# Performance work log

Measured on AMD Instinct MI355X. Metric: run time of the kernel, lower is better.

The kernel has to match this reference:

```python
import jax, jax.numpy as jnp
import numpy as np

N_NODES = 100000
N_EDGES = 1600000
IN_DIM, HID_DIM, OUT_DIM = 128, 64, 64


def setup_inputs() -> dict:
    key = jax.random.key(0)
    k1, k2, k3, k4, k5, k6 = jax.random.split(key, 6)
    x = jax.random.normal(k1, (N_NODES, IN_DIM), dtype=jnp.float32)
    edge_index = jax.random.randint(k2, (2, N_EDGES), 0, N_NODES, dtype=jnp.int64)
    s1 = (2.0 / (IN_DIM + HID_DIM)) ** 0.5
    s2 = (2.0 / (HID_DIM + OUT_DIM)) ** 0.5
    W1 = jax.random.normal(k3, (IN_DIM, HID_DIM), dtype=jnp.float32) * s1
    b1 = jnp.zeros((HID_DIM,), dtype=jnp.float32)
    W2 = jax.random.normal(k4, (HID_DIM, OUT_DIM), dtype=jnp.float32) * s2
    b2 = jnp.zeros((OUT_DIM,), dtype=jnp.float32)
    return {"x": x, "edge_index": edge_index, "W1": W1, "b1": b1, "W2": W2, "b2": b2}


def _gcn_conv(x, src, dst, W, b, num_nodes):
    # linear transform then gather-normalize-scatter (GCN symmetric norm, self-loops added)
    h = x @ W  # [N, F]
    loop = jnp.arange(num_nodes, dtype=src.dtype)
    s = jnp.concatenate([src, loop])
    d = jnp.concatenate([dst, loop])
    ones = jnp.ones(s.shape[0], dtype=h.dtype)
    deg = jax.ops.segment_sum(ones, d, num_segments=num_nodes)
    dinv = jnp.where(deg > 0, jax.lax.rsqrt(jnp.maximum(deg, 1.0)), 0.0)
    norm = dinv[s] * dinv[d]  # [E+N]
    msg = h[s] * norm[:, None]  # gather + scale
    out = jax.ops.segment_sum(msg, d, num_segments=num_nodes)  # scatter-add
    return out + b


def reference(x, edge_index, W1, b1, W2, b2):
    src, dst = edge_index[0], edge_index[1]
    h = jax.nn.relu(_gcn_conv(x, src, dst, W1, b1, N_NODES))
    out = _gcn_conv(h, src, dst, W2, b2, N_NODES)
    return out
```

## Files before the change

kernel.cpp:

```cpp
#include <hip/hip_runtime.h>
#include <hip/hip_bf16.h>


#define FDIM 64
#define NPB  128
#define MAXB1 800

static __device__ __forceinline__ unsigned short f2bf(float f) {
    unsigned int u = __float_as_uint(f);
    unsigned int r = 0x7FFFu + ((u >> 16) & 1u);
    return (unsigned short)((u + r) >> 16);
}
static __device__ __forceinline__ float lof(unsigned int u) {
    return __uint_as_float(u << 16);
}
static __device__ __forceinline__ float hif(unsigned int u) {
    return __uint_as_float(u & 0xFFFF0000u);
}

__global__ __launch_bounds__(256) void bucket_hist(const int* __restrict__ dst, int E,
                                                   int B1, int chunk, int B0,
                                                   int* __restrict__ H) {
    __shared__ int hist[MAXB1];
    const int blk = blockIdx.x, t = threadIdx.x;
    for (int i = t; i < B1; i += 256) hist[i] = 0;
    __syncthreads();
    const int beg = blk * chunk, end = min(E, beg + chunk);
    for (int e = beg + t; e < end; e += 256) atomicAdd(&hist[dst[e] >> 7], 1);
    __syncthreads();
    for (int i = t; i < B1; i += 256) H[i * B0 + blk] = hist[i];
}

__global__ __launch_bounds__(256) void scanA(const int* __restrict__ a, int S,
                                             int* __restrict__ bs) {
    __shared__ int s[256];
    const int blk = blockIdx.x, t = threadIdx.x;
    const int base = blk * 2048 + t * 8;
    int sum = 0;
    #pragma unroll
    for (int j = 0; j < 8; ++j) { int idx = base + j; if (idx < S) sum += a[idx]; }
    s[t] = sum;
    __syncthreads();
    for (int off = 128; off > 0; off >>= 1) {
        if (t < off) s[t] += s[t + off];
        __syncthreads();
    }
    if (t == 0) bs[blk] = s[0];
}

__global__ __launch_bounds__(512) void scanB(int* __restrict__ bs, int nB) {
    __shared__ int s[512];
    const int t = threadIdx.x;
    int v = (t < nB) ? bs[t] : 0;
    s[t] = v;
    __syncthreads();
    for (int off = 1; off < 512; off <<= 1) {
        int x = s[t];
        int y = (t >= off) ? s[t - off] : 0;
        __syncthreads();
        s[t] = x + y;
        __syncthreads();
    }
    if (t < nB) bs[t] = s[t] - v;
}

__global__ __launch_bounds__(256) void scanC(int* __restrict__ a, int S,
                                             const int* __restrict__ bs) {
    __shared__ int s[256];
    const int blk = blockIdx.x, t = threadIdx.x;
    const int base = blk * 2048 + t * 8;
    int v[8];
    int sum = 0;
    #pragma unroll
    for (int j = 0; j < 8; ++j) { int idx = base + j; v[j] = (idx < S) ? a[idx] : 0; sum += v[j]; }
    s[t] = sum;
    __syncthreads();
    const int own = sum;
    for (int off = 1; off < 256; off <<= 1) {
        int x = s[t];
        int y = (t >= off) ? s[t - off] : 0;
        __syncthreads();
        s[t] = x + y;
        __syncthreads();
    }
    int run = bs[blk] + s[t] - own;
    #pragma unroll
    for (int j = 0; j < 8; ++j) { int idx = base + j; if (idx < S) a[idx] = run; run += v[j]; }
}

__global__ __launch_bounds__(256) void bucket_scatter(const int* __restrict__ src,
                                                      const int* __restrict__ dst,
                                                      int E, int B1, int chunk, int B0,
                                                      const int* __restrict__ Hs,
                                                      int* __restrict__ pairs) {
    __shared__ int cur[MAXB1];
    const int blk = blockIdx.x, t = threadIdx.x;
    for (int i = t; i < B1; i += 256) cur[i] = Hs[i * B0 + blk];
    __syncthreads();
    const int beg = blk * chunk, end = min(E, beg + chunk);
    for (int e = beg + t; e < end; e += 256) {
        int d = dst[e];
        int pos = atomicAdd(&cur[d >> 7], 1);
        pairs[pos] = ((d & 127) << 17) | src[e];
    }
}

__global__ __launch_bounds__(256) void bucket_csr(const int* __restrict__ pairs,
                                                  const int* __restrict__ Hs,
                                                  int B0, int E, int N,
                                                  float* __restrict__ dinv,
                                                  int* __restrict__ rowStart,
                                                  int* __restrict__ srcSorted) {
    __shared__ int hist[NPB], pref[NPB], cur[NPB];
    const int b = blockIdx.x, t = threadIdx.x;
    const int B1 = gridDim.x;
    const int vbase = b * NPB;
    const int nv = min(NPB, N - vbase);
    const int estart = Hs[b * B0];
    const int eend = (b + 1 < B1) ? Hs[(b + 1) * B0] : E;

    if (t < NPB) hist[t] = 0;
    __syncthreads();
    for (int e = estart + t; e < eend; e += 256)
        atomicAdd(&hist[pairs[e] >> 17], 1);
    __syncthreads();

    if (t < NPB) pref[t] = hist[t];
    __syncthreads();
    for (int off = 1; off < NPB; off <<= 1) {
        int v = 0;
        if (t < NPB && t >= off) v = pref[t - off];
        __syncthreads();
        if (t < NPB) pref[t] += v;
        __syncthreads();
    }
    if (t < nv) {
        int ex = pref[t] - hist[t];
        rowStart[vbase + t] = estart + ex;
        dinv[vbase + t] = rsqrtf((float)(hist[t] + 1));
        cur[t] = estart + ex;
    }
    if (b == B1 - 1 && t == 0) rowStart[N] = E;
    __syncthreads();
    for (int e = estart + t; e < eend; e += 256) {
        int p = pairs[e];
        int pos = atomicAdd(&cur[p >> 17], 1);
        srcSorted[pos] = p & 0x1FFFF;
    }
}

template <int K>
__global__ __launch_bounds__(256) void gemm_scale(const float* __restrict__ X,
                                                  const float* __restrict__ W,
                                                  const float* __restrict__ dinv,
                                                  unsigned short* __restrict__ G, int N) {
    __shared__ float Wl[K * FDIM];
    const int t = threadIdx.x;
    {
        const float4* Wv  = reinterpret_cast<const float4*>(W);
        float4*       Wlv = reinterpret_cast<float4*>(Wl);
        #pragma unroll
        for (int i = 0; i < (K * FDIM) / (256 * 4); ++i)
            Wlv[i * 256 + t] = Wv[i * 256 + t];
    }
    __syncthreads();

    const int r   = t >> 2;
    const int q   = t & 3;
    const int row = blockIdx.x * 64 + r;
    if (row >= N) return;

    const float4* xr  = reinterpret_cast<const float4*>(X + (size_t)row * K);
    const float4* wlq = reinterpret_cast<const float4*>(Wl) + q * 4;

    float acc[16];
    #pragma unroll
    for (int i = 0; i < 16; ++i) acc[i] = 0.f;

    #pragma unroll 2
    for (int k4 = 0; k4 < K / 4; ++k4) {
        float4 xv = xr[k4];
        float xs[4] = {xv.x, xv.y, xv.z, xv.w};
        #pragma unroll
        for (int j = 0; j < 4; ++j) {
            const float4* wrow = wlq + (size_t)(4 * k4 + j) * 16;
            float4 w0 = wrow[0], w1 = wrow[1], w2 = wrow[2], w3 = wrow[3];
            float xk = xs[j];
            acc[ 0] += xk * w0.x; acc[ 1] += xk * w0.y; acc[ 2] += xk * w0.z; acc[ 3] += xk * w0.w;
            acc[ 4] += xk * w1.x; acc[ 5] += xk * w1.y; acc[ 6] += xk * w1.z; acc[ 7] += xk * w1.w;
            acc[ 8] += xk * w2.x; acc[ 9] += xk * w2.y; acc[10] += xk * w2.z; acc[11] += xk * w2.w;
            acc[12] += xk * w3.x; acc[13] += xk * w3.y; acc[14] += xk * w3.z; acc[15] += xk * w3.w;
        }
    }

    const float dv = dinv[row];
    unsigned int p[8];
    #pragma unroll
    for (int i = 0; i < 8; ++i) {
        unsigned int lo = f2bf(acc[2 * i] * dv);
        unsigned int hi = f2bf(acc[2 * i + 1] * dv);
        p[i] = lo | (hi << 16);
    }
    uint4* gout = reinterpret_cast<uint4*>(G + (size_t)row * FDIM + q * 16);
    gout[0] = make_uint4(p[0], p[1], p[2], p[3]);
    gout[1] = make_uint4(p[4], p[5], p[6], p[7]);
}

#define GATHER2(ii, uu, off)  int ii = srcSorted[eb + 2*(off)]; \
                              unsigned int uu = Gu[(size_t)ii * 32 + fl];

__global__ __launch_bounds__(256, 4) void aggregate(const unsigned int* __restrict__ Gu,
                                                    const int* __restrict__ rowStart,
                                                    const int* __restrict__ srcSorted,
                                                    const float* __restrict__ dinv,
                                                    const float* __restrict__ bias,
                                                    float* __restrict__ OUT, int N, int doRelu) {
    const int lane   = threadIdx.x & 63;
    const int half   = lane >> 5;
    const int fl     = lane & 31;
    const int waveId = blockIdx.x * (blockDim.x >> 6) + (threadIdx.x >> 6);
    const int nWaves = gridDim.x * (blockDim.x >> 6);
    const float2 bv  = reinterpret_cast<const float2*>(bias)[fl];

    for (int v = waveId; v < N; v += nWaves) {
        const int beg = rowStart[v];
        const int end = rowStart[v + 1];

        unsigned int su = 0;
        if (half == 0) su = Gu[(size_t)v * 32 + fl];
        float ax = lof(su), ay = hif(su);

        int e = beg;
        for (; e + 16 <= end; e += 16) {
            const int eb = e + half;
            GATHER2(i0, u0, 0) GATHER2(i1, u1, 1) GATHER2(i2, u2, 2) GATHER2(i3, u3, 3)
            GATHER2(i4, u4, 4) GATHER2(i5, u5, 5) GATHER2(i6, u6, 6) GATHER2(i7, u7, 7)
            ax += ((lof(u0) + lof(u1)) + (lof(u2) + lof(u3)))
                + ((lof(u4) + lof(u5)) + (lof(u6) + lof(u7)));
            ay += ((hif(u0) + hif(u1)) + (hif(u2) + hif(u3)))
                + ((hif(u4) + hif(u5)) + (hif(u6) + hif(u7)));
        }
        int rem = end - e;
        if (rem >= 8) {
            const int eb = e + half;
            GATHER2(i0, u0, 0) GATHER2(i1, u1, 1) GATHER2(i2, u2, 2) GATHER2(i3, u3, 3)
            ax += (lof(u0) + lof(u1)) + (lof(u2) + lof(u3));
            ay += (hif(u0) + hif(u1)) + (hif(u2) + hif(u3));
            e += 8; rem -= 8;
        }
        if (rem >= 4) {
            const int eb = e + half;
            GATHER2(i0, u0, 0) GATHER2(i1, u1, 1)
            ax += lof(u0) + lof(u1);
            ay += hif(u0) + hif(u1);
            e += 4; rem -= 4;
        }
        if (rem >= 2) {
            const int eb = e + half;
            GATHER2(i0, u0, 0)
            ax += lof(u0);
            ay += hif(u0);
            e += 2; rem -= 2;
        }
        if (rem) {
            int i0 = srcSorted[e];
            unsigned int u0 = 0;
            if (half == 0) u0 = Gu[(size_t)i0 * 32 + fl];
            ax += lof(u0);
            ay += hif(u0);
        }

        ax += __shfl_xor(ax, 32, 64);
        ay += __shfl_xor(ay, 32, 64);

        const float dv = dinv[v];
        float2 r;
        r.x = ax * dv + bv.x;
        r.y = ay * dv + bv.y;
        if (doRelu) { r.x = fmaxf(r.x, 0.f); r.y = fmaxf(r.y, 0.f); }
        if (half == 0)
            reinterpret_cast<float2*>(OUT + (size_t)v * FDIM)[fl] = r;
    }
}

extern "C" void kernel_launch(void* const* d_in, const int* in_sizes, int n_in,
                              void* d_out, int out_size, void* d_ws, size_t ws_size,
                              hipStream_t stream) {
    const float* x     = (const float*)d_in[0];
    const int*   edges = (const int*)d_in[1];
    const float* W1    = (const float*)d_in[2];
    const float* b1    = (const float*)d_in[3];
    const float* W2    = (const float*)d_in[4];
    const float* b2    = (const float*)d_in[5];
    float*       out   = (float*)d_out;

    const int N = in_sizes[0] / 128;
    const int E = in_sizes[1] / 2;
    const int* srcIdx = edges;
    const int* dstIdx = edges + E;

    const int B1 = (N + NPB - 1) / NPB;
    const int B0 = 256;
    const int chunk = (E + B0 - 1) / B0;
    const int S  = B1 * B0;
    const int nSB = (S + 2047) / 2048;

    char* ws = (char*)d_ws;
    size_t off = 0;
    auto alloc = [&](size_t bytes) { char* p = ws + off; off = (off + bytes + 255) & ~(size_t)255; return p; };
    float* dinv      = (float*)alloc((size_t)N * 4);
    int*   H         = (int*)  alloc((size_t)S * 4);
    int*   blockSums = (int*)  alloc(512 * 4);
    int*   rowStart  = (int*)  alloc((size_t)(N + 1) * 4);
    int*   srcSorted = (int*)  alloc((size_t)E * 4);
    unsigned short* g1 = (unsigned short*)alloc((size_t)N * FDIM * 2);
    float* x2        = (float*)alloc((size_t)N * FDIM * 4);
    int*   pairs     = (int*)x2;
    unsigned short* g2 = g1;

    const int gT = (N + 63) / 64;

    bucket_hist   <<<B0, 256, 0, stream>>>(dstIdx, E, B1, chunk, B0, H);
    scanA         <<<nSB, 256, 0, stream>>>(H, S, blockSums);
    scanB         <<<1, 512, 0, stream>>>(blockSums, nSB);
    scanC         <<<nSB, 256, 0, stream>>>(H, S, blockSums);
    bucket_scatter<<<B0, 256, 0, stream>>>(srcIdx, dstIdx, E, B1, chunk, B0, H, pairs);
    bucket_csr    <<<B1, 256, 0, stream>>>(pairs, H, B0, E, N, dinv, rowStart, srcSorted);

    gemm_scale<128><<<gT, 256, 0, stream>>>(x,  W1, dinv, g1, N);
    aggregate      <<<2048, 256, 0, stream>>>((const unsigned int*)g1, rowStart, srcSorted, dinv, b1, x2, N, 1);
    gemm_scale<64> <<<gT, 256, 0, stream>>>(x2, W2, dinv, g2, N);
    aggregate      <<<2048, 256, 0, stream>>>((const unsigned int*)g2, rowStart, srcSorted, dinv, b2, out, N, 0);
}
```

Measured before the change: 200.4 us.

## Retile gemm_scale to 4 rows x 8 columns per thread with 128-row blocks

The per-thread tile in the dense transform kernel changes from 1 row x 16 columns to 4 rows x 8 columns, and each block now covers 128 rows. Each weight value loaded from LDS is reused across four rows, which cuts LDS traffic per FMA, and a minimum-occupancy launch bound is added. Each thread now reads four X rows with strided float4 loads, which may coalesce less well. Out-of-range row indices are clamped and their stores guarded for the tail.

```diff
diff --git a/kernel.cpp b/kernel.cpp
--- a/kernel.cpp
+++ b/kernel.cpp
@@ -150,10 +150,10 @@
 }
 
 template <int K>
-__global__ __launch_bounds__(256) void gemm_scale(const float* __restrict__ X,
-                                                  const float* __restrict__ W,
-                                                  const float* __restrict__ dinv,
-                                                  unsigned short* __restrict__ G, int N) {
+__global__ __launch_bounds__(256, 4) void gemm_scale(const float* __restrict__ X,
+                                                     const float* __restrict__ W,
+                                                     const float* __restrict__ dinv,
+                                                     unsigned short* __restrict__ G, int N) {
     __shared__ float Wl[K * FDIM];
     const int t = threadIdx.x;
     {
@@ -165,45 +165,60 @@
     }
     __syncthreads();
 
-    const int r   = t >> 2;
-    const int q   = t & 3;
-    const int row = blockIdx.x * 64 + r;
-    if (row >= N) return;
-
-    const float4* xr  = reinterpret_cast<const float4*>(X + (size_t)row * K);
-    const float4* wlq = reinterpret_cast<const float4*>(Wl) + q * 4;
-
-    float acc[16];
-    #pragma unroll
-    for (int i = 0; i < 16; ++i) acc[i] = 0.f;
+    const int cq = t & 7;
+    const int rg = t >> 3;
+    const int r0 = blockIdx.x * 128 + rg * 4;
+    if (r0 >= N) return;
+
+    const int rA = r0;
+    const int rB = min(r0 + 1, N - 1);
+    const int rC = min(r0 + 2, N - 1);
+    const int rD = min(r0 + 3, N - 1);
+    const float4* xrA = reinterpret_cast<const float4*>(X + (size_t)rA * K);
+    const float4* xrB = reinterpret_cast<const float4*>(X + (size_t)rB * K);
+    const float4* xrC = reinterpret_cast<const float4*>(X + (size_t)rC * K);
+    const float4* xrD = reinterpret_cast<const float4*>(X + (size_t)rD * K);
+
+    float acc[4][8];
+    #pragma unroll
+    for (int i = 0; i < 4; ++i)
+        #pragma unroll
+        for (int c = 0; c < 8; ++c) acc[i][c] = 0.f;
 
     #pragma unroll 2
     for (int k4 = 0; k4 < K / 4; ++k4) {
-        float4 xv = xr[k4];
-        float xs[4] = {xv.x, xv.y, xv.z, xv.w};
+        float4 xv0 = xrA[k4], xv1 = xrB[k4], xv2 = xrC[k4], xv3 = xrD[k4];
+        float xs0[4] = {xv0.x, xv0.y, xv0.z, xv0.w};
+        float xs1[4] = {xv1.x, xv1.y, xv1.z, xv1.w};
+        float xs2[4] = {xv2.x, xv2.y, xv2.z, xv2.w};
+        float xs3[4] = {xv3.x, xv3.y, xv3.z, xv3.w};
         #pragma unroll
         for (int j = 0; j < 4; ++j) {
-            const float4* wrow = wlq + (size_t)(4 * k4 + j) * 16;
-            float4 w0 = wrow[0], w1 = wrow[1], w2 = wrow[2], w3 = wrow[3];
-            float xk = xs[j];
-            acc[ 0] += xk * w0.x; acc[ 1] += xk * w0.y; acc[ 2] += xk * w0.z; acc[ 3] += xk * w0.w;
-            acc[ 4] += xk * w1.x; acc[ 5] += xk * w1.y; acc[ 6] += xk * w1.z; acc[ 7] += xk * w1.w;
-            acc[ 8] += xk * w2.x; acc[ 9] += xk * w2.y; acc[10] += xk * w2.z; acc[11] += xk * w2.w;
-            acc[12] += xk * w3.x; acc[13] += xk * w3.y; acc[14] += xk * w3.z; acc[15] += xk * w3.w;
-        }
-    }
-
-    const float dv = dinv[row];
-    unsigned int p[8];
-    #pragma unroll
-    for (int i = 0; i < 8; ++i) {
-        unsigned int lo = f2bf(acc[2 * i] * dv);
-        unsigned int hi = f2bf(acc[2 * i + 1] * dv);
-        p[i] = lo | (hi << 16);
-    }
-    uint4* gout = reinterpret_cast<uint4*>(G + (size_t)row * FDIM + q * 16);
-    gout[0] = make_uint4(p[0], p[1], p[2], p[3]);
-    gout[1] = make_uint4(p[4], p[5], p[6], p[7]);
+            const float4* wp = reinterpret_cast<const float4*>(Wl + (size_t)(4 * k4 + j) * FDIM + cq * 8);
+            float4 w0 = wp[0], w1 = wp[1];
+            float wv[8] = {w0.x, w0.y, w0.z, w0.w, w1.x, w1.y, w1.z, w1.w};
+            #pragma unroll
+            for (int c = 0; c < 8; ++c) {
+                acc[0][c] += xs0[j] * wv[c];
+                acc[1][c] += xs1[j] * wv[c];
+                acc[2][c] += xs2[j] * wv[c];
+                acc[3][c] += xs3[j] * wv[c];
+            }
+        }
+    }
+
+    #pragma unroll
+    for (int i = 0; i < 4; ++i) {
+        const int r = r0 + i;
+        if (r < N) {
+            const float dv = dinv[r];
+            unsigned int p0 = f2bf(acc[i][0] * dv) | (f2bf(acc[i][1] * dv) << 16);
+            unsigned int p1 = f2bf(acc[i][2] * dv) | (f2bf(acc[i][3] * dv) << 16);
+            unsigned int p2 = f2bf(acc[i][4] * dv) | (f2bf(acc[i][5] * dv) << 16);
+            unsigned int p3 = f2bf(acc[i][6] * dv) | (f2bf(acc[i][7] * dv) << 16);
+            *reinterpret_cast<uint4*>(G + (size_t)r * FDIM + cq * 8) = make_uint4(p0, p1, p2, p3);
+        }
+    }
 }
 
 #define GATHER2(ii, uu, off)  int ii = srcSorted[eb + 2*(off)]; \
@@ -318,7 +333,7 @@
     int*   pairs     = (int*)x2;
     unsigned short* g2 = g1;
 
-    const int gT = (N + 63) / 64;
+    const int gT = (N + 127) / 128;
 
     bucket_hist   <<<B0, 256, 0, stream>>>(dstIdx, E, B1, chunk, B0, H);
     scanA         <<<nSB, 256, 0, stream>>>(H, S, blockSums);
```

Result: faster. 192.0 us (-4.2%).

## Replace scalar FP32 GEMM with bf16 MFMA 16x16x32 persistent-wave kernel

Applied to the files above, without the earlier changes.

Rewrites the dense transform as a persistent-wave kernel. Each wave holds W in registers as bf16 fragments and processes 16-row slabs with mfma_f32_16x16x32_bf16. The inputs X and W are rounded to bf16 before the multiply, which adds precision loss. Output stores become 2-byte scattered writes instead of 16-byte vector stores. The goal is to cut ALU time in the GEMM stages.

```diff
diff --git a/kernel.cpp b/kernel.cpp
--- a/kernel.cpp
+++ b/kernel.cpp
@@ -5,6 +5,9 @@
 #define FDIM 64
 #define NPB  128
 #define MAXB1 800
+
+typedef __attribute__((ext_vector_type(8))) short bf16x8;
+typedef __attribute__((ext_vector_type(4))) float f32x4;
 
 static __device__ __forceinline__ unsigned short f2bf(float f) {
     unsigned int u = __float_as_uint(f);
@@ -150,60 +153,73 @@
 }
 
 template <int K>
-__global__ __launch_bounds__(256) void gemm_scale(const float* __restrict__ X,
-                                                  const float* __restrict__ W,
-                                                  const float* __restrict__ dinv,
-                                                  unsigned short* __restrict__ G, int N) {
-    __shared__ float Wl[K * FDIM];
-    const int t = threadIdx.x;
-    {
-        const float4* Wv  = reinterpret_cast<const float4*>(W);
-        float4*       Wlv = reinterpret_cast<float4*>(Wl);
-        #pragma unroll
-        for (int i = 0; i < (K * FDIM) / (256 * 4); ++i)
-            Wlv[i * 256 + t] = Wv[i * 256 + t];
-    }
-    __syncthreads();
-
-    const int r   = t >> 2;
-    const int q   = t & 3;
-    const int row = blockIdx.x * 64 + r;
-    if (row >= N) return;
-
-    const float4* xr  = reinterpret_cast<const float4*>(X + (size_t)row * K);
-    const float4* wlq = reinterpret_cast<const float4*>(Wl) + q * 4;
-
-    float acc[16];
+__global__ __launch_bounds__(256, 2) void gemm_mfma(const float* __restrict__ X,
+                                                    const float* __restrict__ W,
+                                                    const float* __restrict__ dinv,
+                                                    unsigned short* __restrict__ G, int N) {
+    const int lane = threadIdx.x & 63;
+    const int lr   = lane & 15;
+    const int lg   = lane >> 4;
+    const int wid  = (blockIdx.x * blockDim.x + threadIdx.x) >> 6;
+    const int nW   = (gridDim.x * blockDim.x) >> 6;
+    constexpr int NS = K / 32;
+
+    bf16x8 bf[NS][4];
     #pragma unroll
-    for (int i = 0; i < 16; ++i) acc[i] = 0.f;
-
-    #pragma unroll 2
-    for (int k4 = 0; k4 < K / 4; ++k4) {
-        float4 xv = xr[k4];
-        float xs[4] = {xv.x, xv.y, xv.z, xv.w};
-        #pragma unroll
-        for (int j = 0; j < 4; ++j) {
-            const float4* wrow = wlq + (size_t)(4 * k4 + j) * 16;
-            float4 w0 = wrow[0], w1 = wrow[1], w2 = wrow[2], w3 = wrow[3];
-            float xk = xs[j];
-            acc[ 0] += xk * w0.x; acc[ 1] += xk * w0.y; acc[ 2] += xk * w0.z; acc[ 3] += xk * w0.w;
-            acc[ 4] += xk * w1.x; acc[ 5] += xk * w1.y; acc[ 6] += xk * w1.z; acc[ 7] += xk * w1.w;
-            acc[ 8] += xk * w2.x; acc[ 9] += xk * w2.y; acc[10] += xk * w2.z; acc[11] += xk * w2.w;
-            acc[12] += xk * w3.x; acc[13] += xk * w3.y; acc[14] += xk * w3.z; acc[15] += xk * w3.w;
-        }
-    }
-
-    const float dv = dinv[row];
-    unsigned int p[8];
-    #pragma unroll
-    for (int i = 0; i < 8; ++i) {
-        unsigned int lo = f2bf(acc[2 * i] * dv);
-        unsigned int hi = f2bf(acc[2 * i + 1] * dv);
-        p[i] = lo | (hi << 16);
-    }
-    uint4* gout = reinterpret_cast<uint4*>(G + (size_t)row * FDIM + q * 16);
-    gout[0] = make_uint4(p[0], p[1], p[2], p[3]);
-    gout[1] = make_uint4(p[4], p[5], p[6], p[7]);
+    for (int s = 0; s < NS; ++s) {
+        #pragma unroll
+        for (int c = 0; c < 4; ++c) {
+            const float* wp = W + (size_t)(s * 32 + lg * 8) * FDIM + c * 16 + lr;
+            bf16x8 v;
+            #pragma unroll
+            for (int j = 0; j < 8; ++j) v[j] = (short)f2bf(wp[(size_t)j * FDIM]);
+            bf[s][c] = v;
+        }
+    }
+
+    const int nSlab = N >> 4;
+    for (int sl = wid; sl < nSlab; sl += nW) {
+        const int row0 = sl << 4;
+
+        bf16x8 af[NS];
+        const float* xp = X + (size_t)(row0 + lr) * K + lg * 8;
+        #pragma unroll
+        for (int s = 0; s < NS; ++s) {
+            float4 x0 = *reinterpret_cast<const float4*>(xp + s * 32);
+            float4 x1 = *reinterpret_cast<const float4*>(xp + s * 32 + 4);
+            bf16x8 v;
+            v[0] = (short)f2bf(x0.x); v[1] = (short)f2bf(x0.y);
+            v[2] = (short)f2bf(x0.z); v[3] = (short)f2bf(x0.w);
+            v[4] = (short)f2bf(x1.x); v[5] = (short)f2bf(x1.y);
+            v[6] = (short)f2bf(x1.z); v[7] = (short)f2bf(x1.w);
+            af[s] = v;
+        }
+
+        f32x4 acc[4];
+        #pragma unroll
+        for (int c = 0; c < 4; ++c) acc[c] = (f32x4){0.f, 0.f, 0.f, 0.f};
+
+        #pragma unroll
+        for (int s = 0; s < NS; ++s) {
+            #pragma unroll
+            for (int c = 0; c < 4; ++c)
+                acc[c] = __builtin_amdgcn_mfma_f32_16x16x32_bf16(af[s], bf[s][c], acc[c], 0, 0, 0);
+        }
+
+        const int rb = row0 + lg * 4;
+        const float dv0 = dinv[rb + 0];
+        const float dv1 = dinv[rb + 1];
+        const float dv2 = dinv[rb + 2];
+        const float dv3 = dinv[rb + 3];
+        #pragma unroll
+        for (int c = 0; c < 4; ++c) {
+            unsigned short* gp = G + (size_t)rb * FDIM + c * 16 + lr;
+            gp[0 * FDIM] = f2bf(acc[c][0] * dv0);
+            gp[1 * FDIM] = f2bf(acc[c][1] * dv1);
+            gp[2 * FDIM] = f2bf(acc[c][2] * dv2);
+            gp[3 * FDIM] = f2bf(acc[c][3] * dv3);
+        }
+    }
 }
 
 #define GATHER2(ii, uu, off)  int ii = srcSorted[eb + 2*(off)]; \
@@ -318,8 +334,6 @@
     int*   pairs     = (int*)x2;
     unsigned short* g2 = g1;
 
-    const int gT = (N + 63) / 64;
-
     bucket_hist   <<<B0, 256, 0, stream>>>(dstIdx, E, B1, chunk, B0, H);
     scanA         <<<nSB, 256, 0, stream>>>(H, S, blockSums);
     scanB         <<<1, 512, 0, stream>>>(blockSums, nSB);
@@ -327,8 +341,8 @@
     bucket_scatter<<<B0, 256, 0, stream>>>(srcIdx, dstIdx, E, B1, chunk, B0, H, pairs);
     bucket_csr    <<<B1, 256, 0, stream>>>(pairs, H, B0, E, N, dinv, rowStart, srcSorted);
 
-    gemm_scale<128><<<gT, 256, 0, stream>>>(x,  W1, dinv, g1, N);
-    aggregate      <<<2048, 256, 0, stream>>>((const unsigned int*)g1, rowStart, srcSorted, dinv, b1, x2, N, 1);
-    gemm_scale<64> <<<gT, 256, 0, stream>>>(x2, W2, dinv, g2, N);
-    aggregate      <<<2048, 256, 0, stream>>>((const unsigned int*)g2, rowStart, srcSorted, dinv, b2, out, N, 0);
-}
+    gemm_mfma<128><<<768, 256, 0, stream>>>(x,  W1, dinv, g1, N);
+    aggregate     <<<2048, 256, 0, stream>>>((const unsigned int*)g1, rowStart, srcSorted, dinv, b1, x2, N, 1);
+    gemm_mfma<64> <<<768, 256, 0, stream>>>(x2, W2, dinv, g2, N);
+    aggregate     <<<2048, 256, 0, stream>>>((const unsigned int*)g2, rowStart, srcSorted, dinv, b2, out, N, 0);
+}
```

Result: faster. 162.9 us (-18.7%).
